# Optimization experiments

Measured on AMD Instinct MI355X. Metric: run time of the kernel, lower is better.

## Reference

```python
import jax, jax.numpy as jnp
import numpy as np

N = 2048
D_T = 256; D_F = 256
E_T = 32; E_F = 32; E_C = 128
C = 5; Q = 512


def setup_inputs() -> dict:
    key = jax.random.key(0)
    ks = jax.random.split(key, 12)
    # full graph minus self-loops, row-major (matches dense_to_sparse ordering)
    r, c = np.meshgrid(np.arange(N), np.arange(N), indexing='ij')
    m = r != c
    edge_index = jnp.asarray(np.stack([r[m], c[m]]), dtype=jnp.int32)  # [2, N*(N-1)]
    E = edge_index.shape[1]
    s = 0.02
    return {
        'time_features': jax.random.normal(ks[0], (N, D_T), jnp.float32),
        'edge_index': edge_index,
        'time_edge_weight': jax.random.uniform(ks[1], (E,), jnp.float32),
        'freq_features': jax.random.normal(ks[2], (N, D_F), jnp.float32),
        'freq_edge_weight': jax.random.uniform(ks[3], (E,), jnp.float32),
        'labels': jax.random.randint(ks[4], (N,), 0, C, jnp.int32),
        'num_classes': C,
        'query_size': Q,
        'Wt': jax.random.normal(ks[5], (D_T, E_T), jnp.float32) * s,
        'bt': jnp.zeros((E_T,), jnp.float32),
        'Wf': jax.random.normal(ks[6], (D_F, E_F), jnp.float32) * s,
        'bf': jnp.zeros((E_F,), jnp.float32),
        'Wc': jax.random.normal(ks[7], (E_T + E_F + C, E_C), jnp.float32) * s,
        'bc': jnp.zeros((E_C,), jnp.float32),
        'Wo': jax.random.normal(ks[8], (E_C, C), jnp.float32) * s,
        'bo': jnp.zeros((C,), jnp.float32),
    }


def _gcn(x, A, W, b):
    # torch_geometric GCNConv: D^{-1/2}(A + I)D^{-1/2} (X W) + b
    n = A.shape[0]
    Ah = A + jnp.eye(n, dtype=A.dtype)
    deg = Ah.sum(axis=1)
    dis = jnp.where(deg > 0, jax.lax.rsqrt(deg), 0.0)
    return (dis[:, None] * Ah * dis[None, :]) @ (x @ W) + b


def reference(time_features, edge_index, time_edge_weight, freq_features,
              freq_edge_weight, labels, num_classes, query_size,
              Wt, bt, Wf, bf, Wc, bc, Wo, bo):
    n = time_features.shape[0]
    lrelu = lambda z: jax.nn.leaky_relu(z, 0.01)

    def dense_adj(w):  # A[dst, src] = w
        return jnp.zeros((n, n), w.dtype).at[edge_index[1], edge_index[0]].add(w)

    te = lrelu(_gcn(time_features, dense_adj(time_edge_weight), Wt, bt))
    fe = lrelu(_gcn(freq_features, dense_adj(freq_edge_weight), Wf, bf))

    # to_one_hot: one_hot[:n - query_size, labels] = 1 -> support rows get 1 in
    # every column that appears anywhere in `labels`
    cols = jnp.zeros((num_classes,), te.dtype).at[labels].set(1.0)
    rowmask = (jnp.arange(n) < (n - query_size)).astype(te.dtype)
    one_hot = rowmask[:, None] * cols[None, :]

    feats = jnp.concatenate([te, fe, one_hot], axis=-1)  # [n, E_T+E_F+C]

    # graph_construction (no_grad in original): 1 / (L1 distance over the
    # non-one-hot dims + 1e-5), zero diagonal
    fd = jax.lax.stop_gradient(feats[:, : feats.shape[1] - num_classes])
    dist = jnp.sum(jnp.abs(fd[:, None, :] - fd[None, :, :]), axis=-1)  # [n, n]
    Aw = (1.0 / (dist + 1e-5)) * (1.0 - jnp.eye(n, dtype=feats.dtype))

    emb = lrelu(_gcn(feats, Aw, Wc, bc))
    return emb @ Wo + bo
```

## Files before the change

kernel.cpp:

```cpp
#include <hip/hip_runtime.h>
#include <hip/hip_bf16.h>

#define N 2048
#define NM1 2047
#define DT 256
#define ET 32
#define EC 128
#define NC 5
#define FS 80
#define FD 69
#define KC_ET 16
#define KC_EC 16

typedef __hip_bfloat16 bf16;
typedef unsigned short u16;
typedef float f32x4 __attribute__((ext_vector_type(4)));
typedef __bf16 bf16x8 __attribute__((ext_vector_type(8)));

__device__ inline u16 bf16_rne(float x){
    unsigned int b = __float_as_uint(x);
    b += 0x7fffu + ((b >> 16) & 1u);
    return (u16)(b >> 16);
}
__device__ inline float bf16_to_f(u16 h){
    return __uint_as_float(((unsigned int)h) << 16);
}

__device__ inline f32x4 mfma16x16x32(bf16x8 a, bf16x8 b, f32x4 c){
    return __builtin_amdgcn_mfma_f32_16x16x32_bf16(a, b, c, 0, 0, 0);
}

__global__ __launch_bounds__(256) void k_deg_label_xw(const float* __restrict__ tw,
                                                      const float* __restrict__ fw,
                                                      const int* __restrict__ labels,
                                                      const float* __restrict__ Xt,
                                                      const float* __restrict__ Wt,
                                                      const float* __restrict__ Xf,
                                                      const float* __restrict__ Wf,
                                                      float* __restrict__ degT,
                                                      float* __restrict__ degF,
                                                      float* __restrict__ cols,
                                                      float* __restrict__ Yt,
                                                      float* __restrict__ Yf){
    int b = blockIdx.x;
    int t = threadIdx.x;
    if (b < 512){
        int p = (b & 7)*256 + t;
        if (p >= NM1) return;
        int s0 = (b >> 3)*32;
        float lowT=0.f, highT=0.f, lowF=0.f, highF=0.f;
        #pragma unroll 8
        for (int r = 0; r < 32; ++r){
            int s = s0 + r;
            float vt = tw[(size_t)s*NM1 + p];
            float vf = fw[(size_t)s*NM1 + p];
            if (s <= p){ highT += vt; highF += vf; }
            else       { lowT  += vt; lowF  += vf; }
        }
        atomicAdd(&degT[p],   lowT);
        atomicAdd(&degF[p],   lowF);
        atomicAdd(&degT[p+1], highT);
        atomicAdd(&degF[p+1], highF);
        return;
    }
    if (b == 512){
        __shared__ float lc[NC];
        if (t < NC) lc[t] = 0.f;
        __syncthreads();
        for (int i = t; i < N; i += 256){
            int l = labels[i];
            if (l >= 0 && l < NC) lc[l] = 1.f;
        }
        __syncthreads();
        if (t < NC) cols[t] = lc[t];
        return;
    }
    int idx = b - 513;
    const float* X = (idx & 256) ? Xf : Xt;
    const float* W = (idx & 256) ? Wf : Wt;
    float*       Y = (idx & 256) ? Yf : Yt;
    __shared__ float Ws[DT*ET];
    __shared__ float Xs[8*DT];
    for (int j = t; j < DT*ET; j += 256) Ws[j] = W[j];
    int i0 = (idx & 255)*8;
    for (int j = t; j < 8*DT; j += 256) Xs[j] = X[(size_t)i0*DT + j];
    __syncthreads();
    int r = t >> 5, f = t & 31;
    const float* xr = Xs + r*DT;
    float acc = 0.f;
    #pragma unroll 8
    for (int d = 0; d < DT; ++d) acc += xr[d]*Ws[d*ET+f];
    Y[(size_t)(i0+r)*ET+f] = acc;
}

__global__ __launch_bounds__(256) void k_agg_et(const float* __restrict__ tw,
                                                const float* __restrict__ fw,
                                                const float* __restrict__ Yt,
                                                const float* __restrict__ Yf,
                                                const float* __restrict__ degT,
                                                const float* __restrict__ degF,
                                                float* __restrict__ Pt,
                                                float* __restrict__ Pf){
    __shared__ float Ast[64*68];
    __shared__ float Asf[64*68];
    __shared__ float Zst[64*ET];
    __shared__ float Zsf[64*ET];
    int t = threadIdx.x;
    int i0 = blockIdx.x*64;
    int kc = blockIdx.y;
    int k0 = kc*128;
    int g  = t >> 7;
    int tt = t & 127;
    int ig = tt >> 3, fg = tt & 7;
    int r0 = ig*4, c0 = fg*4;
    const float* As = g ? Asf : Ast;
    const float* Zs = g ? Zsf : Zst;
    float acc[4][4];
    #pragma unroll
    for (int u=0;u<4;++u)
        #pragma unroll
        for (int v=0;v<4;++v) acc[u][v]=0.f;

    for (int kt = 0; kt < 2; ++kt){
        int kb = k0 + kt*64;
        #pragma unroll
        for (int e = 0; e < 16; ++e){
            int id = t + e*256;
            int k_l = id >> 6, i_l = id & 63;
            int k = kb + k_l;
            int gi = i0 + i_l;
            float vt, vf;
            if (gi == k){ vt = 0.f; vf = 0.f; }
            else {
                size_t base = (size_t)k*NM1 + gi - (gi > k ? 1 : 0);
                vt = tw[base]; vf = fw[base];
            }
            Ast[k_l*68 + i_l] = vt;
            Asf[k_l*68 + i_l] = vf;
        }
        #pragma unroll
        for (int e = 0; e < 2; ++e){
            int id = t + e*256;
            int row = id >> 3;
            int c4  = (id & 7)*4;
            float rdT = rsqrtf(1.f + degT[kb+row]);
            float rdF = rsqrtf(1.f + degF[kb+row]);
            float4 yt = *(const float4*)&Yt[(size_t)(kb+row)*ET + c4];
            float4 yf = *(const float4*)&Yf[(size_t)(kb+row)*ET + c4];
            yt.x*=rdT; yt.y*=rdT; yt.z*=rdT; yt.w*=rdT;
            yf.x*=rdF; yf.y*=rdF; yf.z*=rdF; yf.w*=rdF;
            *(float4*)&Zst[row*ET + c4] = yt;
            *(float4*)&Zsf[row*ET + c4] = yf;
        }
        __syncthreads();
        for (int k = 0; k < 64; ++k){
            float4 a = *(const float4*)&As[k*68 + r0];
            float4 z = *(const float4*)&Zs[k*ET + c0];
            const float* ap = (const float*)&a;
            const float* zp = (const float*)&z;
            #pragma unroll
            for (int u = 0; u < 4; ++u)
                #pragma unroll
                for (int v = 0; v < 4; ++v)
                    acc[u][v] += ap[u]*zp[v];
        }
        __syncthreads();
    }
    float* P = g ? Pf : Pt;
    #pragma unroll
    for (int u = 0; u < 4; ++u){
        size_t ii = (size_t)(i0 + r0 + u);
        float4 o;
        float* po = (float*)&o;
        #pragma unroll
        for (int v = 0; v < 4; ++v) po[v]=acc[u][v];
        *(float4*)&P[(size_t)kc*(N*ET) + ii*ET + c0] = o;
    }
}

__global__ __launch_bounds__(256) void k_feats_epi(const float* __restrict__ Pt,
                                                   const float* __restrict__ Pf,
                                                   const float* __restrict__ Yt,
                                                   const float* __restrict__ Yf,
                                                   const float* __restrict__ degT,
                                                   const float* __restrict__ degF,
                                                   const float* __restrict__ bt,
                                                   const float* __restrict__ bfv,
                                                   const float* __restrict__ cols,
                                                   const int* __restrict__ qsize,
                                                   float* __restrict__ feats){
    int idx = blockIdx.x*256 + threadIdx.x;
    int i = idx >> 6;
    int f = idx & 63;
    float s, rd, b;
    if (f < ET){
        rd = rsqrtf(1.f + degT[i]);
        s = rd*Yt[(size_t)i*ET + f];
        #pragma unroll
        for (int kc = 0; kc < KC_ET; ++kc) s += Pt[(size_t)kc*(N*ET) + (size_t)i*ET + f];
        b = bt[f];
    } else {
        int g = f - ET;
        rd = rsqrtf(1.f + degF[i]);
        s = rd*Yf[(size_t)i*ET + g];
        #pragma unroll
        for (int kc = 0; kc < KC_ET; ++kc) s += Pf[(size_t)kc*(N*ET) + (size_t)i*ET + g];
        b = bfv[g];
    }
    float v = rd*s + b;
    feats[(size_t)i*FS + f] = v > 0.f ? v : 0.01f*v;
    if (f < NC){
        int nsup = N - qsize[0];
        feats[(size_t)i*FS + 2*ET + f] = (i < nsup) ? cols[f] : 0.f;
    }
}

__global__ __launch_bounds__(256) void k_build_aw(const float* __restrict__ feats,
                                                  u16* __restrict__ Aw_hi,
                                                  u16* __restrict__ Aw_lo,
                                                  float* __restrict__ dsum){
    __shared__ float fiT[64*68];
    __shared__ float fjT[64*68];
    int t = threadIdx.x;
    int i0 = blockIdx.x*64, j0 = blockIdx.y*64;
    {
        int row = t >> 2;
        int cb  = (t & 3)*16;
        const float4* si = (const float4*)(feats + (size_t)(i0+row)*FS + cb);
        const float4* sj = (const float4*)(feats + (size_t)(j0+row)*FS + cb);
        #pragma unroll
        for (int s = 0; s < 4; ++s){
            float4 v = si[s];
            float4 w = sj[s];
            int c = cb + s*4;
            fiT[(c+0)*68+row]=v.x; fiT[(c+1)*68+row]=v.y; fiT[(c+2)*68+row]=v.z; fiT[(c+3)*68+row]=v.w;
            fjT[(c+0)*68+row]=w.x; fjT[(c+1)*68+row]=w.y; fjT[(c+2)*68+row]=w.z; fjT[(c+3)*68+row]=w.w;
        }
    }
    __syncthreads();
    int tx = t & 15, ty = t >> 4;
    float acc[4][4];
    #pragma unroll
    for (int u=0;u<4;++u)
        #pragma unroll
        for (int v=0;v<4;++v) acc[u][v]=0.f;
    for (int d = 0; d < 64; ++d){
        float4 a4 = *(const float4*)&fiT[d*68 + ty*4];
        float4 b4 = *(const float4*)&fjT[d*68 + tx*4];
        const float* ap = (const float*)&a4;
        const float* bp = (const float*)&b4;
        #pragma unroll
        for (int u = 0; u < 4; ++u)
            #pragma unroll
            for (int v = 0; v < 4; ++v)
                acc[u][v] += fabsf(ap[u]-bp[v]);
    }
    #pragma unroll
    for (int u = 0; u < 4; ++u){
        int gi = i0 + ty*4 + u;
        float po[4];
        u16 hh[4], ll[4];
        #pragma unroll
        for (int v = 0; v < 4; ++v){
            int gj = j0 + tx*4 + v;
            float w = (gi==gj) ? 1.0f : 1.0f/(acc[u][v] + 1e-5f);
            po[v] = w;
            u16 h = bf16_rne(w);
            hh[v] = h;
            ll[v] = bf16_rne(w - bf16_to_f(h));
        }
        uint2 ph, pl;
        ph.x = (unsigned)hh[0] | ((unsigned)hh[1]<<16);
        ph.y = (unsigned)hh[2] | ((unsigned)hh[3]<<16);
        pl.x = (unsigned)ll[0] | ((unsigned)ll[1]<<16);
        pl.y = (unsigned)ll[2] | ((unsigned)ll[3]<<16);
        *(uint2*)&Aw_hi[(size_t)gi*N + j0 + tx*4] = ph;
        *(uint2*)&Aw_lo[(size_t)gi*N + j0 + tx*4] = pl;
        float rs = (po[0]+po[1]) + (po[2]+po[3]);
        rs += __shfl_xor(rs, 1);
        rs += __shfl_xor(rs, 2);
        rs += __shfl_xor(rs, 4);
        rs += __shfl_xor(rs, 8);
        if (tx == 0) atomicAdd(&dsum[gi], rs);
    }
}

__global__ __launch_bounds__(256) void k_featswc(const float* __restrict__ feats,
                                                 const float* __restrict__ Wc,
                                                 const float* __restrict__ dsum,
                                                 u16* __restrict__ ZcT_hi,
                                                 u16* __restrict__ ZcT_lo){
    __shared__ float Wcs[FD*EC];
    __shared__ float fr[8][FD+3];
    __shared__ float zb[128][12];
    int t = threadIdx.x;
    for (int idx = t; idx < FD*EC; idx += 256) Wcs[idx] = Wc[idx];
    int i0 = blockIdx.x*8;
    for (int idx = t; idx < 8*FD; idx += 256){
        int r = idx / FD;
        int c = idx - r*FD;
        fr[r][c] = feats[(size_t)(i0+r)*FS + c];
    }
    __syncthreads();
    int f  = t & 127;
    int rh = t >> 7;
    for (int rr = 0; rr < 4; ++rr){
        int r = rh*4 + rr;
        float acc = 0.f;
        #pragma unroll
        for (int d = 0; d < FD; ++d) acc += fr[r][d]*Wcs[d*EC+f];
        int i = i0 + r;
        zb[f][r] = rsqrtf(dsum[i])*acc;
    }
    __syncthreads();
    int p = rh, f2 = f;
    float4 v0 = *(const float4*)&zb[f2][0];
    float4 v1 = *(const float4*)&zb[f2][4];
    float vv[8] = {v0.x, v0.y, v0.z, v0.w, v1.x, v1.y, v1.z, v1.w};
    u16 s[8];
    #pragma unroll
    for (int j = 0; j < 8; ++j){
        u16 h = bf16_rne(vv[j]);
        s[j] = p ? bf16_rne(vv[j] - bf16_to_f(h)) : h;
    }
    uint4 pk;
    pk.x = (unsigned)s[0] | ((unsigned)s[1]<<16);
    pk.y = (unsigned)s[2] | ((unsigned)s[3]<<16);
    pk.z = (unsigned)s[4] | ((unsigned)s[5]<<16);
    pk.w = (unsigned)s[6] | ((unsigned)s[7]<<16);
    u16* dst = p ? ZcT_lo : ZcT_hi;
    *(uint4*)&dst[(size_t)f2*N + i0] = pk;
}

__global__ __launch_bounds__(256) void k_agg_ec(const u16* __restrict__ Aw_hi,
                                                const u16* __restrict__ Aw_lo,
                                                const u16* __restrict__ ZcT_hi,
                                                const u16* __restrict__ ZcT_lo,
                                                float* __restrict__ Pe){
    __shared__ u16 Ah[64*72];
    __shared__ u16 Al[64*72];
    __shared__ u16 Zh[128*72];
    __shared__ u16 Zl[128*72];
    int t = threadIdx.x;
    int w  = t >> 6;
    int l  = t & 63;
    int lr = l & 15;
    int lg = l >> 4;
    int i0 = blockIdx.x*64;
    int kb0 = blockIdx.y*128;
    f32x4 acc[8];
    #pragma unroll
    for (int tt = 0; tt < 8; ++tt) acc[tt] = (f32x4){0.f, 0.f, 0.f, 0.f};

    for (int sub = 0; sub < 2; ++sub){
        int kbs = kb0 + sub*64;
        #pragma unroll
        for (int e = 0; e < 2; ++e){
            int id = t + e*256;
            int row = id >> 3, ch = (id & 7)*8;
            uint4 vh = *(const uint4*)&Aw_hi[(size_t)(i0+row)*N + kbs + ch];
            uint4 vl = *(const uint4*)&Aw_lo[(size_t)(i0+row)*N + kbs + ch];
            *(uint4*)&Ah[row*72 + ch] = vh;
            *(uint4*)&Al[row*72 + ch] = vl;
        }
        #pragma unroll
        for (int e = 0; e < 4; ++e){
            int id = t + e*256;
            int row = id >> 3, ch = (id & 7)*8;
            uint4 vh = *(const uint4*)&ZcT_hi[(size_t)row*N + kbs + ch];
            uint4 vl = *(const uint4*)&ZcT_lo[(size_t)row*N + kbs + ch];
            *(uint4*)&Zh[row*72 + ch] = vh;
            *(uint4*)&Zl[row*72 + ch] = vl;
        }
        __syncthreads();
        #pragma unroll
        for (int ks = 0; ks < 2; ++ks){
            int aoff = (w*16 + lr)*72 + ks*32 + lg*8;
            bf16x8 aH = *(const bf16x8*)&Ah[aoff];
            bf16x8 aL = *(const bf16x8*)&Al[aoff];
            #pragma unroll
            for (int tt = 0; tt < 8; ++tt){
                int zoff = (tt*16 + lr)*72 + ks*32 + lg*8;
                bf16x8 bH = *(const bf16x8*)&Zh[zoff];
                bf16x8 bL = *(const bf16x8*)&Zl[zoff];
                acc[tt] = mfma16x16x32(aH, bH, acc[tt]);
                acc[tt] = mfma16x16x32(aL, bH, acc[tt]);
                acc[tt] = mfma16x16x32(aH, bL, acc[tt]);
            }
        }
        __syncthreads();
    }
    float* pout = Pe + (size_t)blockIdx.y*((size_t)N*EC);
    #pragma unroll
    for (int tt = 0; tt < 8; ++tt){
        #pragma unroll
        for (int r = 0; r < 4; ++r){
            int gi = i0 + w*16 + lg*4 + r;
            pout[(size_t)gi*EC + tt*16 + lr] = acc[tt][r];
        }
    }
}

__global__ __launch_bounds__(256) void k_embfinal(const float* __restrict__ Pe,
                                                  const float* __restrict__ dsum,
                                                  const float* __restrict__ bc,
                                                  const float* __restrict__ Wo,
                                                  const float* __restrict__ bo,
                                                  float* __restrict__ out){
    __shared__ float vs[2][EC];
    __shared__ float Wos[EC*NC];
    __shared__ float bos[NC];
    int t = threadIdx.x;
    for (int idx = t; idx < EC*NC; idx += 256) Wos[idx] = Wo[idx];
    if (t < NC) bos[t] = bo[t];
    int rr = t >> 7, f = t & 127;
    int i = blockIdx.x*2 + rr;
    size_t idx = (size_t)i*EC + f;
    float s = 0.f;
    #pragma unroll
    for (int kc = 0; kc < KC_EC; ++kc) s += Pe[(size_t)kc*(N*EC) + idx];
    float v = rsqrtf(dsum[i])*s + bc[f];
    vs[rr][f] = v > 0.f ? v : 0.01f*v;
    __syncthreads();
    if (t < 2*NC){
        int r = t / NC;
        int c = t - r*NC;
        float a = bos[c];
        #pragma unroll 8
        for (int f2 = 0; f2 < EC; ++f2) a += vs[r][f2]*Wos[f2*NC+c];
        out[(size_t)(blockIdx.x*2 + r)*NC + c] = a;
    }
}

extern "C" void kernel_launch(void* const* d_in, const int* in_sizes, int n_in,
                              void* d_out, int out_size, void* d_ws, size_t ws_size,
                              hipStream_t stream) {
    const float* time_features = (const float*)d_in[0];
    const float* tw            = (const float*)d_in[2];
    const float* freq_features = (const float*)d_in[3];
    const float* fw            = (const float*)d_in[4];
    const int*   labels        = (const int*)d_in[5];
    const int*   qsize         = (const int*)d_in[7];
    const float* Wt  = (const float*)d_in[8];
    const float* bt  = (const float*)d_in[9];
    const float* Wf  = (const float*)d_in[10];
    const float* bfv = (const float*)d_in[11];
    const float* Wc  = (const float*)d_in[12];
    const float* bc  = (const float*)d_in[13];
    const float* Wo  = (const float*)d_in[14];
    const float* bo  = (const float*)d_in[15];
    float* out = (float*)d_out;

    float* ws    = (float*)d_ws;
    float* Yt    = ws;
    float* Yf    = Yt + (size_t)N*ET;
    float* Zc    = Yf + (size_t)N*ET;
    float* degT  = Zc + (size_t)N*EC;
    float* degF  = degT + N;
    float* dsum  = degF + N;
    float* colsb = dsum + N;
    float* feats = colsb + 8;
    float* Aw    = feats + (size_t)N*FS;
    float* Pt    = Aw + (size_t)N*N;
    float* Pf    = Pt + (size_t)KC_ET*N*ET;
    float* Pe    = Pf + (size_t)KC_ET*N*ET;

    u16* Aw_hi  = (u16*)Aw;
    u16* Aw_lo  = Aw_hi + (size_t)N*N;
    u16* ZcT_hi = (u16*)Zc;
    u16* ZcT_lo = ZcT_hi + (size_t)N*EC;

    hipMemsetAsync(degT, 0, 3*N*sizeof(float), stream);
    k_deg_label_xw<<<1025, 256, 0, stream>>>(tw, fw, labels,
                                             time_features, Wt, freq_features, Wf,
                                             degT, degF, colsb, Yt, Yf);
    k_agg_et<<<dim3(N/64, KC_ET), 256, 0, stream>>>(tw, fw, Yt, Yf, degT, degF, Pt, Pf);
    k_feats_epi<<<(N*64)/256, 256, 0, stream>>>(Pt, Pf, Yt, Yf, degT, degF,
                                                bt, bfv, colsb, qsize, feats);
    k_build_aw<<<dim3(N/64, N/64), 256, 0, stream>>>(feats, Aw_hi, Aw_lo, dsum);
    k_featswc<<<N/8, 256, 0, stream>>>(feats, Wc, dsum, ZcT_hi, ZcT_lo);
    k_agg_ec<<<dim3(N/64, KC_EC), 256, 0, stream>>>(Aw_hi, Aw_lo, ZcT_hi, ZcT_lo, Pe);
    k_embfinal<<<N/2, 256, 0, stream>>>(Pe, dsum, bc, Wo, bo, out);
}
```

Before: 199.8 us.

## Fuse split-K GCN aggregations with epilogues, drop partial buffers, use MFMA for first stage

The first-layer aggregation moves from FP32 FMA to split-bf16 MFMA (hi/lo, three products). It drops split-K, so each block covers 16 rows over the full K range, and the bias, leaky-ReLU and feats epilogue are fused in. The second aggregation is likewise made full-K per 16-row block and fused with the final embedding and output projection, removing the Pe partial-sum buffer and two kernel launches. The trade-off is far fewer blocks (256 and 128) with long serial K loops and less parallelism, which could leave much of the GPU idle.

Result: slower. 264.6 us (+32.4%).

```diff
diff --git a/kernel.cpp b/kernel.cpp
--- a/kernel.cpp
+++ b/kernel.cpp
@@ -9,10 +9,7 @@
 #define NC 5
 #define FS 80
 #define FD 69
-#define KC_ET 16
-#define KC_EC 16
-
-typedef __hip_bfloat16 bf16;
+
 typedef unsigned short u16;
 typedef float f32x4 __attribute__((ext_vector_type(4)));
 typedef __bf16 bf16x8 __attribute__((ext_vector_type(8)));
@@ -25,7 +22,6 @@
 __device__ inline float bf16_to_f(u16 h){
     return __uint_as_float(((unsigned int)h) << 16);
 }
-
 __device__ inline f32x4 mfma16x16x32(bf16x8 a, bf16x8 b, f32x4 c){
     return __builtin_amdgcn_mfma_f32_16x16x32_bf16(a, b, c, 0, 0, 0);
 }
@@ -93,125 +89,85 @@
     Y[(size_t)(i0+r)*ET+f] = acc;
 }
 
-__global__ __launch_bounds__(256) void k_agg_et(const float* __restrict__ tw,
-                                                const float* __restrict__ fw,
-                                                const float* __restrict__ Yt,
-                                                const float* __restrict__ Yf,
-                                                const float* __restrict__ degT,
-                                                const float* __restrict__ degF,
-                                                float* __restrict__ Pt,
-                                                float* __restrict__ Pf){
-    __shared__ float Ast[64*68];
-    __shared__ float Asf[64*68];
-    __shared__ float Zst[64*ET];
-    __shared__ float Zsf[64*ET];
+__global__ __launch_bounds__(256) void k_agg_et_full(const float* __restrict__ tw,
+                                                     const float* __restrict__ fw,
+                                                     const float* __restrict__ Yt,
+                                                     const float* __restrict__ Yf,
+                                                     const float* __restrict__ degT,
+                                                     const float* __restrict__ degF,
+                                                     const float* __restrict__ bt,
+                                                     const float* __restrict__ bfv,
+                                                     const float* __restrict__ cols,
+                                                     const int* __restrict__ qsize,
+                                                     float* __restrict__ feats){
+    __shared__ u16 Ah[16*72], Al[16*72];
+    __shared__ u16 Zh[32*72], Zl[32*72];
+    __shared__ float red[256*4];
     int t = threadIdx.x;
-    int i0 = blockIdx.x*64;
-    int kc = blockIdx.y;
-    int k0 = kc*128;
-    int g  = t >> 7;
-    int tt = t & 127;
-    int ig = tt >> 3, fg = tt & 7;
-    int r0 = ig*4, c0 = fg*4;
-    const float* As = g ? Asf : Ast;
-    const float* Zs = g ? Zsf : Zst;
-    float acc[4][4];
-    #pragma unroll
-    for (int u=0;u<4;++u)
-        #pragma unroll
-        for (int v=0;v<4;++v) acc[u][v]=0.f;
-
-    for (int kt = 0; kt < 2; ++kt){
-        int kb = k0 + kt*64;
-        #pragma unroll
-        for (int e = 0; e < 16; ++e){
+    int tile = blockIdx.x >> 1;
+    int g = blockIdx.x & 1;
+    int i0 = tile*16;
+    const float* A   = g ? fw   : tw;
+    const float* Y   = g ? Yf   : Yt;
+    const float* deg = g ? degF : degT;
+    int w = t >> 6, l = t & 63, lr = l & 15, lg = l >> 4;
+    int cf = w & 1, kp = w >> 1;
+    f32x4 acc = {0.f, 0.f, 0.f, 0.f};
+
+    for (int sub = 0; sub < 32; ++sub){
+        int kb = sub*64;
+        #pragma unroll
+        for (int e = 0; e < 4; ++e){
             int id = t + e*256;
-            int k_l = id >> 6, i_l = id & 63;
-            int k = kb + k_l;
-            int gi = i0 + i_l;
-            float vt, vf;
-            if (gi == k){ vt = 0.f; vf = 0.f; }
-            else {
-                size_t base = (size_t)k*NM1 + gi - (gi > k ? 1 : 0);
-                vt = tw[base]; vf = fw[base];
-            }
-            Ast[k_l*68 + i_l] = vt;
-            Asf[k_l*68 + i_l] = vf;
-        }
-        #pragma unroll
-        for (int e = 0; e < 2; ++e){
+            int i_l = id & 15, k_l = id >> 4;
+            int gi = i0 + i_l, k = kb + k_l;
+            float v = 0.f;
+            if (gi != k) v = A[(size_t)k*NM1 + gi - (gi > k ? 1 : 0)];
+            u16 h = bf16_rne(v);
+            Ah[i_l*72 + k_l] = h;
+            Al[i_l*72 + k_l] = bf16_rne(v - bf16_to_f(h));
+        }
+        #pragma unroll
+        for (int e = 0; e < 8; ++e){
             int id = t + e*256;
-            int row = id >> 3;
-            int c4  = (id & 7)*4;
-            float rdT = rsqrtf(1.f + degT[kb+row]);
-            float rdF = rsqrtf(1.f + degF[kb+row]);
-            float4 yt = *(const float4*)&Yt[(size_t)(kb+row)*ET + c4];
-            float4 yf = *(const float4*)&Yf[(size_t)(kb+row)*ET + c4];
-            yt.x*=rdT; yt.y*=rdT; yt.z*=rdT; yt.w*=rdT;
-            yf.x*=rdF; yf.y*=rdF; yf.z*=rdF; yf.w*=rdF;
-            *(float4*)&Zst[row*ET + c4] = yt;
-            *(float4*)&Zsf[row*ET + c4] = yf;
-        }
-        __syncthreads();
-        for (int k = 0; k < 64; ++k){
-            float4 a = *(const float4*)&As[k*68 + r0];
-            float4 z = *(const float4*)&Zs[k*ET + c0];
-            const float* ap = (const float*)&a;
-            const float* zp = (const float*)&z;
-            #pragma unroll
-            for (int u = 0; u < 4; ++u)
-                #pragma unroll
-                for (int v = 0; v < 4; ++v)
-                    acc[u][v] += ap[u]*zp[v];
-        }
-        __syncthreads();
-    }
-    float* P = g ? Pf : Pt;
-    #pragma unroll
-    for (int u = 0; u < 4; ++u){
-        size_t ii = (size_t)(i0 + r0 + u);
-        float4 o;
-        float* po = (float*)&o;
-        #pragma unroll
-        for (int v = 0; v < 4; ++v) po[v]=acc[u][v];
-        *(float4*)&P[(size_t)kc*(N*ET) + ii*ET + c0] = o;
-    }
-}
-
-__global__ __launch_bounds__(256) void k_feats_epi(const float* __restrict__ Pt,
-                                                   const float* __restrict__ Pf,
-                                                   const float* __restrict__ Yt,
-                                                   const float* __restrict__ Yf,
-                                                   const float* __restrict__ degT,
-                                                   const float* __restrict__ degF,
-                                                   const float* __restrict__ bt,
-                                                   const float* __restrict__ bfv,
-                                                   const float* __restrict__ cols,
-                                                   const int* __restrict__ qsize,
-                                                   float* __restrict__ feats){
-    int idx = blockIdx.x*256 + threadIdx.x;
-    int i = idx >> 6;
-    int f = idx & 63;
-    float s, rd, b;
-    if (f < ET){
-        rd = rsqrtf(1.f + degT[i]);
-        s = rd*Yt[(size_t)i*ET + f];
-        #pragma unroll
-        for (int kc = 0; kc < KC_ET; ++kc) s += Pt[(size_t)kc*(N*ET) + (size_t)i*ET + f];
-        b = bt[f];
-    } else {
-        int g = f - ET;
-        rd = rsqrtf(1.f + degF[i]);
-        s = rd*Yf[(size_t)i*ET + g];
-        #pragma unroll
-        for (int kc = 0; kc < KC_ET; ++kc) s += Pf[(size_t)kc*(N*ET) + (size_t)i*ET + g];
-        b = bfv[g];
-    }
-    float v = rd*s + b;
-    feats[(size_t)i*FS + f] = v > 0.f ? v : 0.01f*v;
-    if (f < NC){
+            int f = id & 31, k_l = id >> 5;
+            float rd = rsqrtf(1.f + deg[kb + k_l]);
+            float v = rd * Y[(size_t)(kb+k_l)*ET + f];
+            u16 h = bf16_rne(v);
+            Zh[f*72 + k_l] = h;
+            Zl[f*72 + k_l] = bf16_rne(v - bf16_to_f(h));
+        }
+        __syncthreads();
+        int aoff = lr*72 + kp*32 + lg*8;
+        int boff = (cf*16 + lr)*72 + kp*32 + lg*8;
+        bf16x8 aH = *(const bf16x8*)&Ah[aoff];
+        bf16x8 aL = *(const bf16x8*)&Al[aoff];
+        bf16x8 bH = *(const bf16x8*)&Zh[boff];
+        bf16x8 bL = *(const bf16x8*)&Zl[boff];
+        acc = mfma16x16x32(aH, bH, acc);
+        acc = mfma16x16x32(aL, bH, acc);
+        acc = mfma16x16x32(aH, bL, acc);
+        __syncthreads();
+    }
+    *(f32x4*)&red[t*4] = acc;
+    __syncthreads();
+    if (w < 2){
+        f32x4 o = *(const f32x4*)&red[(t+128)*4];
+        int fl = cf*16 + lr;
+        float bb = g ? bfv[fl] : bt[fl];
+        #pragma unroll
+        for (int j = 0; j < 4; ++j){
+            int i = i0 + lg*4 + j;
+            float rd = rsqrtf(1.f + deg[i]);
+            float s = rd*Y[(size_t)i*ET + fl] + acc[j] + o[j];
+            float v = rd*s + bb;
+            feats[(size_t)i*FS + g*ET + fl] = v > 0.f ? v : 0.01f*v;
+        }
+    }
+    if (g == 0 && t < 16*NC){
+        int r = t / NC, c = t - r*NC;
         int nsup = N - qsize[0];
-        feats[(size_t)i*FS + 2*ET + f] = (i < nsup) ? cols[f] : 0.f;
+        feats[(size_t)(i0+r)*FS + 2*ET + c] = (i0+r < nsup) ? cols[c] : 0.f;
     }
 }
 
@@ -332,103 +288,76 @@
     *(uint4*)&dst[(size_t)f2*N + i0] = pk;
 }
 
-__global__ __launch_bounds__(256) void k_agg_ec(const u16* __restrict__ Aw_hi,
-                                                const u16* __restrict__ Aw_lo,
-                                                const u16* __restrict__ ZcT_hi,
-                                                const u16* __restrict__ ZcT_lo,
-                                                float* __restrict__ Pe){
-    __shared__ u16 Ah[64*72];
-    __shared__ u16 Al[64*72];
-    __shared__ u16 Zh[128*72];
-    __shared__ u16 Zl[128*72];
+__global__ __launch_bounds__(256) void k_agg_ec_full(const u16* __restrict__ Aw_hi,
+                                                     const u16* __restrict__ Aw_lo,
+                                                     const u16* __restrict__ ZcT_hi,
+                                                     const u16* __restrict__ ZcT_lo,
+                                                     const float* __restrict__ dsum,
+                                                     const float* __restrict__ bc,
+                                                     const float* __restrict__ Wo,
+                                                     const float* __restrict__ bo,
+                                                     float* __restrict__ out){
+    __shared__ u16 Ah[16*72], Al[16*72];
+    __shared__ u16 Zh[128*72], Zl[128*72];
+    __shared__ float vs[16*128];
     int t = threadIdx.x;
-    int w  = t >> 6;
-    int l  = t & 63;
-    int lr = l & 15;
-    int lg = l >> 4;
-    int i0 = blockIdx.x*64;
-    int kb0 = blockIdx.y*128;
-    f32x4 acc[8];
-    #pragma unroll
-    for (int tt = 0; tt < 8; ++tt) acc[tt] = (f32x4){0.f, 0.f, 0.f, 0.f};
-
-    for (int sub = 0; sub < 2; ++sub){
-        int kbs = kb0 + sub*64;
-        #pragma unroll
-        for (int e = 0; e < 2; ++e){
-            int id = t + e*256;
-            int row = id >> 3, ch = (id & 7)*8;
-            uint4 vh = *(const uint4*)&Aw_hi[(size_t)(i0+row)*N + kbs + ch];
-            uint4 vl = *(const uint4*)&Aw_lo[(size_t)(i0+row)*N + kbs + ch];
-            *(uint4*)&Ah[row*72 + ch] = vh;
-            *(uint4*)&Al[row*72 + ch] = vl;
+    int i0 = blockIdx.x*16;
+    int w = t >> 6, l = t & 63, lr = l & 15, lg = l >> 4;
+    f32x4 acc0 = {0.f,0.f,0.f,0.f}, acc1 = {0.f,0.f,0.f,0.f};
+
+    for (int sub = 0; sub < 32; ++sub){
+        int kb = sub*64;
+        {
+            int row = t >> 4, c4 = (t & 15)*4;
+            *(uint2*)&Ah[row*72 + c4] = *(const uint2*)&Aw_hi[(size_t)(i0+row)*N + kb + c4];
+            *(uint2*)&Al[row*72 + c4] = *(const uint2*)&Aw_lo[(size_t)(i0+row)*N + kb + c4];
         }
         #pragma unroll
         for (int e = 0; e < 4; ++e){
             int id = t + e*256;
-            int row = id >> 3, ch = (id & 7)*8;
-            uint4 vh = *(const uint4*)&ZcT_hi[(size_t)row*N + kbs + ch];
-            uint4 vl = *(const uint4*)&ZcT_lo[(size_t)row*N + kbs + ch];
-            *(uint4*)&Zh[row*72 + ch] = vh;
-            *(uint4*)&Zl[row*72 + ch] = vl;
+            int fr = id >> 3, ch = (id & 7)*8;
+            *(uint4*)&Zh[fr*72 + ch] = *(const uint4*)&ZcT_hi[(size_t)fr*N + kb + ch];
+            *(uint4*)&Zl[fr*72 + ch] = *(const uint4*)&ZcT_lo[(size_t)fr*N + kb + ch];
         }
         __syncthreads();
         #pragma unroll
         for (int ks = 0; ks < 2; ++ks){
-            int aoff = (w*16 + lr)*72 + ks*32 + lg*8;
+            int aoff = lr*72 + ks*32 + lg*8;
             bf16x8 aH = *(const bf16x8*)&Ah[aoff];
             bf16x8 aL = *(const bf16x8*)&Al[aoff];
-            #pragma unroll
-            for (int tt = 0; tt < 8; ++tt){
-                int zoff = (tt*16 + lr)*72 + ks*32 + lg*8;
-                bf16x8 bH = *(const bf16x8*)&Zh[zoff];
-                bf16x8 bL = *(const bf16x8*)&Zl[zoff];
-                acc[tt] = mfma16x16x32(aH, bH, acc[tt]);
-                acc[tt] = mfma16x16x32(aL, bH, acc[tt]);
-                acc[tt] = mfma16x16x32(aH, bL, acc[tt]);
-            }
-        }
-        __syncthreads();
-    }
-    float* pout = Pe + (size_t)blockIdx.y*((size_t)N*EC);
+            int b0 = ((w*2+0)*16 + lr)*72 + ks*32 + lg*8;
+            int b1 = ((w*2+1)*16 + lr)*72 + ks*32 + lg*8;
+            bf16x8 bH0 = *(const bf16x8*)&Zh[b0];
+            bf16x8 bL0 = *(const bf16x8*)&Zl[b0];
+            bf16x8 bH1 = *(const bf16x8*)&Zh[b1];
+            bf16x8 bL1 = *(const bf16x8*)&Zl[b1];
+            acc0 = mfma16x16x32(aH, bH0, acc0);
+            acc0 = mfma16x16x32(aL, bH0, acc0);
+            acc0 = mfma16x16x32(aH, bL0, acc0);
+            acc1 = mfma16x16x32(aH, bH1, acc1);
+            acc1 = mfma16x16x32(aL, bH1, acc1);
+            acc1 = mfma16x16x32(aH, bL1, acc1);
+        }
+        __syncthreads();
+    }
     #pragma unroll
-    for (int tt = 0; tt < 8; ++tt){
-        #pragma unroll
-        for (int r = 0; r < 4; ++r){
-            int gi = i0 + w*16 + lg*4 + r;
-            pout[(size_t)gi*EC + tt*16 + lr] = acc[tt][r];
-        }
-    }
-}
-
-__global__ __launch_bounds__(256) void k_embfinal(const float* __restrict__ Pe,
-                                                  const float* __restrict__ dsum,
-                                                  const float* __restrict__ bc,
-                                                  const float* __restrict__ Wo,
-                                                  const float* __restrict__ bo,
-                                                  float* __restrict__ out){
-    __shared__ float vs[2][EC];
-    __shared__ float Wos[EC*NC];
-    __shared__ float bos[NC];
-    int t = threadIdx.x;
-    for (int idx = t; idx < EC*NC; idx += 256) Wos[idx] = Wo[idx];
-    if (t < NC) bos[t] = bo[t];
-    int rr = t >> 7, f = t & 127;
-    int i = blockIdx.x*2 + rr;
-    size_t idx = (size_t)i*EC + f;
-    float s = 0.f;
-    #pragma unroll
-    for (int kc = 0; kc < KC_EC; ++kc) s += Pe[(size_t)kc*(N*EC) + idx];
-    float v = rsqrtf(dsum[i])*s + bc[f];
-    vs[rr][f] = v > 0.f ? v : 0.01f*v;
-    __syncthreads();
-    if (t < 2*NC){
-        int r = t / NC;
-        int c = t - r*NC;
-        float a = bos[c];
+    for (int j = 0; j < 4; ++j){
+        int row = lg*4 + j;
+        float rdv = rsqrtf(dsum[i0+row]);
+        int c0 = (w*2+0)*16 + lr;
+        int c1 = (w*2+1)*16 + lr;
+        float v0 = rdv*acc0[j] + bc[c0];
+        float v1 = rdv*acc1[j] + bc[c1];
+        vs[row*128 + c0] = v0 > 0.f ? v0 : 0.01f*v0;
+        vs[row*128 + c1] = v1 > 0.f ? v1 : 0.01f*v1;
+    }
+    __syncthreads();
+    if (t < 16*NC){
+        int r = t / NC, c = t - r*NC;
+        float a = bo[c];
         #pragma unroll 8
-        for (int f2 = 0; f2 < EC; ++f2) a += vs[r][f2]*Wos[f2*NC+c];
-        out[(size_t)(blockIdx.x*2 + r)*NC + c] = a;
+        for (int f = 0; f < EC; ++f) a += vs[r*128 + f]*Wo[f*NC + c];
+        out[(size_t)(i0 + r)*NC + c] = a;
     }
 }
 
@@ -452,33 +381,29 @@
     float* out = (float*)d_out;
 
     float* ws    = (float*)d_ws;
-    float* Yt    = ws;
-    float* Yf    = Yt + (size_t)N*ET;
-    float* Zc    = Yf + (size_t)N*ET;
-    float* degT  = Zc + (size_t)N*EC;
+    float* degT  = ws;
     float* degF  = degT + N;
     float* dsum  = degF + N;
     float* colsb = dsum + N;
-    float* feats = colsb + 8;
-    float* Aw    = feats + (size_t)N*FS;
-    float* Pt    = Aw + (size_t)N*N;
-    float* Pf    = Pt + (size_t)KC_ET*N*ET;
-    float* Pe    = Pf + (size_t)KC_ET*N*ET;
-
+    float* Yt    = colsb + 8;
+    float* Yf    = Yt + (size_t)N*ET;
+    float* feats = Yf + (size_t)N*ET;
+    float* Zc    = feats + (size_t)N*FS;
+    float* Aw    = Zc + (size_t)N*EC;
+
+    u16* ZcT_hi = (u16*)Zc;
+    u16* ZcT_lo = ZcT_hi + (size_t)N*EC;
     u16* Aw_hi  = (u16*)Aw;
     u16* Aw_lo  = Aw_hi + (size_t)N*N;
-    u16* ZcT_hi = (u16*)Zc;
-    u16* ZcT_lo = ZcT_hi + (size_t)N*EC;
 
     hipMemsetAsync(degT, 0, 3*N*sizeof(float), stream);
     k_deg_label_xw<<<1025, 256, 0, stream>>>(tw, fw, labels,
                                              time_features, Wt, freq_features, Wf,
                                              degT, degF, colsb, Yt, Yf);
-    k_agg_et<<<dim3(N/64, KC_ET), 256, 0, stream>>>(tw, fw, Yt, Yf, degT, degF, Pt, Pf);
-    k_feats_epi<<<(N*64)/256, 256, 0, stream>>>(Pt, Pf, Yt, Yf, degT, degF,
-                                                bt, bfv, colsb, qsize, feats);
+    k_agg_et_full<<<256, 256, 0, stream>>>(tw, fw, Yt, Yf, degT, degF,
+                                           bt, bfv, colsb, qsize, feats);
     k_build_aw<<<dim3(N/64, N/64), 256, 0, stream>>>(feats, Aw_hi, Aw_lo, dsum);
     k_featswc<<<N/8, 256, 0, stream>>>(feats, Wc, dsum, ZcT_hi, ZcT_lo);
-    k_agg_ec<<<dim3(N/64, KC_EC), 256, 0, stream>>>(Aw_hi, Aw_lo, ZcT_hi, ZcT_lo, Pe);
-    k_embfinal<<<N/2, 256, 0, stream>>>(Pe, dsum, bc, Wo, bo, out);
-}
+    k_agg_ec_full<<<128, 256, 0, stream>>>(Aw_hi, Aw_lo, ZcT_hi, ZcT_lo,
+                                           dsum, bc, Wo, bo, out);
+}
```

## Use split-bf16 MFMA for edge aggregation and fuse Aw build with feats·Wc

Applied to the files above, without the earlier changes.

Rewrites the time/frequency adjacency aggregation to use bf16 hi/lo split MFMA instead of scalar FP32 FMAs, reading adjacency directly from global memory into registers. Merges the Aw distance kernel and the feats·Wc kernel into one launch. To allow that merge, the rsqrt(dsum) column scaling moves out of Zc and into k_agg_ec's A-tile load, where each Aw element is recombined, rescaled and re-split. This saves a launch and uses matrix cores, but adds extra conversion ALU work in k_agg_ec, and the 3-term split may slightly change precision.

Result: faster. 191.1 us (-4.4%).

```diff
diff --git a/kernel.cpp b/kernel.cpp
--- a/kernel.cpp
+++ b/kernel.cpp
@@ -12,7 +12,6 @@
 #define KC_ET 16
 #define KC_EC 16
 
-typedef __hip_bfloat16 bf16;
 typedef unsigned short u16;
 typedef float f32x4 __attribute__((ext_vector_type(4)));
 typedef __bf16 bf16x8 __attribute__((ext_vector_type(8)));
@@ -25,7 +24,6 @@
 __device__ inline float bf16_to_f(u16 h){
     return __uint_as_float(((unsigned int)h) << 16);
 }
-
 __device__ inline f32x4 mfma16x16x32(bf16x8 a, bf16x8 b, f32x4 c){
     return __builtin_amdgcn_mfma_f32_16x16x32_bf16(a, b, c, 0, 0, 0);
 }
@@ -93,89 +91,122 @@
     Y[(size_t)(i0+r)*ET+f] = acc;
 }
 
-__global__ __launch_bounds__(256) void k_agg_et(const float* __restrict__ tw,
-                                                const float* __restrict__ fw,
-                                                const float* __restrict__ Yt,
-                                                const float* __restrict__ Yf,
-                                                const float* __restrict__ degT,
-                                                const float* __restrict__ degF,
-                                                float* __restrict__ Pt,
-                                                float* __restrict__ Pf){
-    __shared__ float Ast[64*68];
-    __shared__ float Asf[64*68];
-    __shared__ float Zst[64*ET];
-    __shared__ float Zsf[64*ET];
+__global__ __launch_bounds__(256) void k_agg_et_m(const float* __restrict__ tw,
+                                                  const float* __restrict__ fw,
+                                                  const float* __restrict__ Yt,
+                                                  const float* __restrict__ Yf,
+                                                  const float* __restrict__ degT,
+                                                  const float* __restrict__ degF,
+                                                  float* __restrict__ Pt,
+                                                  float* __restrict__ Pf){
+    __shared__ u16 Zs[2][2][32][136];
     int t = threadIdx.x;
+    int w = t >> 6, l = t & 63, lr = l & 15, lg = l >> 4;
+    int g = w >> 1, wh = w & 1;
     int i0 = blockIdx.x*64;
     int kc = blockIdx.y;
     int k0 = kc*128;
-    int g  = t >> 7;
-    int tt = t & 127;
-    int ig = tt >> 3, fg = tt & 7;
-    int r0 = ig*4, c0 = fg*4;
-    const float* As = g ? Asf : Ast;
-    const float* Zs = g ? Zsf : Zst;
-    float acc[4][4];
+
+    {
+        int f = t >> 3;
+        int kb16 = (t & 7)*16;
+        #pragma unroll
+        for (int gg = 0; gg < 2; ++gg){
+            const float* Y   = gg ? Yf   : Yt;
+            const float* deg = gg ? degF : degT;
+            u16 h8[16], l8[16];
+            #pragma unroll
+            for (int j = 0; j < 16; ++j){
+                int k = k0 + kb16 + j;
+                float rd = rsqrtf(1.f + deg[k]);
+                float v = rd * Y[(size_t)k*ET + f];
+                u16 h = bf16_rne(v);
+                h8[j] = h;
+                l8[j] = bf16_rne(v - bf16_to_f(h));
+            }
+            uint4 pk;
+            pk.x = (unsigned)h8[0] | ((unsigned)h8[1]<<16);
+            pk.y = (unsigned)h8[2] | ((unsigned)h8[3]<<16);
+            pk.z = (unsigned)h8[4] | ((unsigned)h8[5]<<16);
+            pk.w = (unsigned)h8[6] | ((unsigned)h8[7]<<16);
+            *(uint4*)&Zs[gg][0][f][kb16] = pk;
+            pk.x = (unsigned)h8[8] | ((unsigned)h8[9]<<16);
+            pk.y = (unsigned)h8[10] | ((unsigned)h8[11]<<16);
+            pk.z = (unsigned)h8[12] | ((unsigned)h8[13]<<16);
+            pk.w = (unsigned)h8[14] | ((unsigned)h8[15]<<16);
+            *(uint4*)&Zs[gg][0][f][kb16+8] = pk;
+            pk.x = (unsigned)l8[0] | ((unsigned)l8[1]<<16);
+            pk.y = (unsigned)l8[2] | ((unsigned)l8[3]<<16);
+            pk.z = (unsigned)l8[4] | ((unsigned)l8[5]<<16);
+            pk.w = (unsigned)l8[6] | ((unsigned)l8[7]<<16);
+            *(uint4*)&Zs[gg][1][f][kb16] = pk;
+            pk.x = (unsigned)l8[8] | ((unsigned)l8[9]<<16);
+            pk.y = (unsigned)l8[10] | ((unsigned)l8[11]<<16);
+            pk.z = (unsigned)l8[12] | ((unsigned)l8[13]<<16);
+            pk.w = (unsigned)l8[14] | ((unsigned)l8[15]<<16);
+            *(uint4*)&Zs[gg][1][f][kb16+8] = pk;
+        }
+    }
+    __syncthreads();
+
+    const float* A = g ? fw : tw;
+    f32x4 acc[2][2];
     #pragma unroll
-    for (int u=0;u<4;++u)
-        #pragma unroll
-        for (int v=0;v<4;++v) acc[u][v]=0.f;
-
-    for (int kt = 0; kt < 2; ++kt){
-        int kb = k0 + kt*64;
-        #pragma unroll
-        for (int e = 0; e < 16; ++e){
-            int id = t + e*256;
-            int k_l = id >> 6, i_l = id & 63;
-            int k = kb + k_l;
-            int gi = i0 + i_l;
-            float vt, vf;
-            if (gi == k){ vt = 0.f; vf = 0.f; }
-            else {
-                size_t base = (size_t)k*NM1 + gi - (gi > k ? 1 : 0);
-                vt = tw[base]; vf = fw[base];
-            }
-            Ast[k_l*68 + i_l] = vt;
-            Asf[k_l*68 + i_l] = vf;
-        }
-        #pragma unroll
-        for (int e = 0; e < 2; ++e){
-            int id = t + e*256;
-            int row = id >> 3;
-            int c4  = (id & 7)*4;
-            float rdT = rsqrtf(1.f + degT[kb+row]);
-            float rdF = rsqrtf(1.f + degF[kb+row]);
-            float4 yt = *(const float4*)&Yt[(size_t)(kb+row)*ET + c4];
-            float4 yf = *(const float4*)&Yf[(size_t)(kb+row)*ET + c4];
-            yt.x*=rdT; yt.y*=rdT; yt.z*=rdT; yt.w*=rdT;
-            yf.x*=rdF; yf.y*=rdF; yf.z*=rdF; yf.w*=rdF;
-            *(float4*)&Zst[row*ET + c4] = yt;
-            *(float4*)&Zsf[row*ET + c4] = yf;
-        }
-        __syncthreads();
-        for (int k = 0; k < 64; ++k){
-            float4 a = *(const float4*)&As[k*68 + r0];
-            float4 z = *(const float4*)&Zs[k*ET + c0];
-            const float* ap = (const float*)&a;
-            const float* zp = (const float*)&z;
-            #pragma unroll
-            for (int u = 0; u < 4; ++u)
+    for (int fi = 0; fi < 2; ++fi)
+        #pragma unroll
+        for (int ff = 0; ff < 2; ++ff) acc[fi][ff] = (f32x4){0.f,0.f,0.f,0.f};
+
+    for (int sub = 0; sub < 2; ++sub){
+        int kb = k0 + sub*64;
+        #pragma unroll
+        for (int fi = 0; fi < 2; ++fi){
+            int row = i0 + wh*32 + fi*16 + lr;
+            #pragma unroll
+            for (int ks = 0; ks < 2; ++ks){
+                int kbase = kb + ks*32 + lg*8;
+                u16 ah[8], al[8];
                 #pragma unroll
-                for (int v = 0; v < 4; ++v)
-                    acc[u][v] += ap[u]*zp[v];
-        }
-        __syncthreads();
+                for (int j = 0; j < 8; ++j){
+                    int k = kbase + j;
+                    float v = 0.f;
+                    if (row != k) v = A[(size_t)k*NM1 + row - (row > k ? 1 : 0)];
+                    u16 h = bf16_rne(v);
+                    ah[j] = h;
+                    al[j] = bf16_rne(v - bf16_to_f(h));
+                }
+                uint4 pa, pb;
+                pa.x = (unsigned)ah[0] | ((unsigned)ah[1]<<16);
+                pa.y = (unsigned)ah[2] | ((unsigned)ah[3]<<16);
+                pa.z = (unsigned)ah[4] | ((unsigned)ah[5]<<16);
+                pa.w = (unsigned)ah[6] | ((unsigned)ah[7]<<16);
+                pb.x = (unsigned)al[0] | ((unsigned)al[1]<<16);
+                pb.y = (unsigned)al[2] | ((unsigned)al[3]<<16);
+                pb.z = (unsigned)al[4] | ((unsigned)al[5]<<16);
+                pb.w = (unsigned)al[6] | ((unsigned)al[7]<<16);
+                bf16x8 aH = *(bf16x8*)&pa;
+                bf16x8 aL = *(bf16x8*)&pb;
+                int koff = sub*64 + ks*32 + lg*8;
+                #pragma unroll
+                for (int ff = 0; ff < 2; ++ff){
+                    bf16x8 bH = *(const bf16x8*)&Zs[g][0][ff*16+lr][koff];
+                    bf16x8 bL = *(const bf16x8*)&Zs[g][1][ff*16+lr][koff];
+                    acc[fi][ff] = mfma16x16x32(aH, bH, acc[fi][ff]);
+                    acc[fi][ff] = mfma16x16x32(aL, bH, acc[fi][ff]);
+                    acc[fi][ff] = mfma16x16x32(aH, bL, acc[fi][ff]);
+                }
+            }
+        }
     }
     float* P = g ? Pf : Pt;
     #pragma unroll
-    for (int u = 0; u < 4; ++u){
-        size_t ii = (size_t)(i0 + r0 + u);
-        float4 o;
-        float* po = (float*)&o;
-        #pragma unroll
-        for (int v = 0; v < 4; ++v) po[v]=acc[u][v];
-        *(float4*)&P[(size_t)kc*(N*ET) + ii*ET + c0] = o;
-    }
+    for (int fi = 0; fi < 2; ++fi)
+        #pragma unroll
+        for (int ff = 0; ff < 2; ++ff)
+            #pragma unroll
+            for (int r = 0; r < 4; ++r){
+                int gi = i0 + wh*32 + fi*16 + lg*4 + r;
+                P[(size_t)kc*(N*ET) + (size_t)gi*ET + ff*16 + lr] = acc[fi][ff][r];
+            }
 }
 
 __global__ __launch_bounds__(256) void k_feats_epi(const float* __restrict__ Pt,
@@ -215,127 +246,122 @@
     }
 }
 
-__global__ __launch_bounds__(256) void k_build_aw(const float* __restrict__ feats,
-                                                  u16* __restrict__ Aw_hi,
-                                                  u16* __restrict__ Aw_lo,
-                                                  float* __restrict__ dsum){
-    __shared__ float fiT[64*68];
-    __shared__ float fjT[64*68];
+__global__ __launch_bounds__(256) void k_aw_zc(const float* __restrict__ feats,
+                                               const float* __restrict__ Wc,
+                                               u16* __restrict__ Aw_hi,
+                                               u16* __restrict__ Aw_lo,
+                                               u16* __restrict__ ZcT_hi,
+                                               u16* __restrict__ ZcT_lo,
+                                               float* __restrict__ dsum){
+    __shared__ __align__(16) char sm[37632];
     int t = threadIdx.x;
-    int i0 = blockIdx.x*64, j0 = blockIdx.y*64;
+    int b = blockIdx.x;
+    if (b < 1024){
+        float* fiT = (float*)sm;
+        float* fjT = fiT + 64*68;
+        int i0 = (b & 31)*64, j0 = (b >> 5)*64;
+        {
+            int row = t >> 2;
+            int cb  = (t & 3)*16;
+            const float4* si = (const float4*)(feats + (size_t)(i0+row)*FS + cb);
+            const float4* sj = (const float4*)(feats + (size_t)(j0+row)*FS + cb);
+            #pragma unroll
+            for (int s = 0; s < 4; ++s){
+                float4 v = si[s];
+                float4 w = sj[s];
+                int c = cb + s*4;
+                fiT[(c+0)*68+row]=v.x; fiT[(c+1)*68+row]=v.y; fiT[(c+2)*68+row]=v.z; fiT[(c+3)*68+row]=v.w;
+                fjT[(c+0)*68+row]=w.x; fjT[(c+1)*68+row]=w.y; fjT[(c+2)*68+row]=w.z; fjT[(c+3)*68+row]=w.w;
+            }
+        }
+        __syncthreads();
+        int tx = t & 15, ty = t >> 4;
+        float acc[4][4];
+        #pragma unroll
+        for (int u=0;u<4;++u)
+            #pragma unroll
+            for (int v=0;v<4;++v) acc[u][v]=0.f;
+        for (int d = 0; d < 64; ++d){
+            float4 a4 = *(const float4*)&fiT[d*68 + ty*4];
+            float4 b4 = *(const float4*)&fjT[d*68 + tx*4];
+            const float* ap = (const float*)&a4;
+            const float* bp = (const float*)&b4;
+            #pragma unroll
+            for (int u = 0; u < 4; ++u)
+                #pragma unroll
+                for (int v = 0; v < 4; ++v)
+                    acc[u][v] += fabsf(ap[u]-bp[v]);
+        }
+        #pragma unroll
+        for (int u = 0; u < 4; ++u){
+            int gi = i0 + ty*4 + u;
+            float po[4];
+            u16 hh[4], ll[4];
+            #pragma unroll
+            for (int v = 0; v < 4; ++v){
+                int gj = j0 + tx*4 + v;
+                float w = (gi==gj) ? 1.0f : 1.0f/(acc[u][v] + 1e-5f);
+                po[v] = w;
+                u16 h = bf16_rne(w);
+                hh[v] = h;
+                ll[v] = bf16_rne(w - bf16_to_f(h));
+            }
+            uint2 ph, pl;
+            ph.x = (unsigned)hh[0] | ((unsigned)hh[1]<<16);
+            ph.y = (unsigned)hh[2] | ((unsigned)hh[3]<<16);
+            pl.x = (unsigned)ll[0] | ((unsigned)ll[1]<<16);
+            pl.y = (unsigned)ll[2] | ((unsigned)ll[3]<<16);
+            *(uint2*)&Aw_hi[(size_t)gi*N + j0 + tx*4] = ph;
+            *(uint2*)&Aw_lo[(size_t)gi*N + j0 + tx*4] = pl;
+            float rs = (po[0]+po[1]) + (po[2]+po[3]);
+            rs += __shfl_xor(rs, 1);
+            rs += __shfl_xor(rs, 2);
+            rs += __shfl_xor(rs, 4);
+            rs += __shfl_xor(rs, 8);
+            if (tx == 0) atomicAdd(&dsum[gi], rs);
+        }
+        return;
+    }
     {
-        int row = t >> 2;
-        int cb  = (t & 3)*16;
-        const float4* si = (const float4*)(feats + (size_t)(i0+row)*FS + cb);
-        const float4* sj = (const float4*)(feats + (size_t)(j0+row)*FS + cb);
-        #pragma unroll
-        for (int s = 0; s < 4; ++s){
-            float4 v = si[s];
-            float4 w = sj[s];
-            int c = cb + s*4;
-            fiT[(c+0)*68+row]=v.x; fiT[(c+1)*68+row]=v.y; fiT[(c+2)*68+row]=v.z; fiT[(c+3)*68+row]=v.w;
-            fjT[(c+0)*68+row]=w.x; fjT[(c+1)*68+row]=w.y; fjT[(c+2)*68+row]=w.z; fjT[(c+3)*68+row]=w.w;
-        }
-    }
-    __syncthreads();
-    int tx = t & 15, ty = t >> 4;
-    float acc[4][4];
-    #pragma unroll
-    for (int u=0;u<4;++u)
-        #pragma unroll
-        for (int v=0;v<4;++v) acc[u][v]=0.f;
-    for (int d = 0; d < 64; ++d){
-        float4 a4 = *(const float4*)&fiT[d*68 + ty*4];
-        float4 b4 = *(const float4*)&fjT[d*68 + tx*4];
-        const float* ap = (const float*)&a4;
-        const float* bp = (const float*)&b4;
-        #pragma unroll
-        for (int u = 0; u < 4; ++u)
-            #pragma unroll
-            for (int v = 0; v < 4; ++v)
-                acc[u][v] += fabsf(ap[u]-bp[v]);
-    }
-    #pragma unroll
-    for (int u = 0; u < 4; ++u){
-        int gi = i0 + ty*4 + u;
-        float po[4];
+        float* Wcs = (float*)sm;
+        float* fr  = Wcs + FD*EC;
+        int idx = b - 1024;
+        int i0 = idx*8;
+        for (int j = t; j < FD*EC; j += 256) Wcs[j] = Wc[j];
+        for (int j = t; j < 8*FD; j += 256){
+            int r = j / FD;
+            int c = j - r*FD;
+            fr[r*72 + c] = feats[(size_t)(i0+r)*FS + c];
+        }
+        __syncthreads();
+        int f  = t & 127;
+        int rh = t >> 7;
         u16 hh[4], ll[4];
         #pragma unroll
-        for (int v = 0; v < 4; ++v){
-            int gj = j0 + tx*4 + v;
-            float w = (gi==gj) ? 1.0f : 1.0f/(acc[u][v] + 1e-5f);
-            po[v] = w;
-            u16 h = bf16_rne(w);
-            hh[v] = h;
-            ll[v] = bf16_rne(w - bf16_to_f(h));
+        for (int rr = 0; rr < 4; ++rr){
+            int r = rh*4 + rr;
+            float acc = 0.f;
+            #pragma unroll
+            for (int d = 0; d < FD; ++d) acc += fr[r*72+d]*Wcs[d*EC+f];
+            u16 h = bf16_rne(acc);
+            hh[rr] = h;
+            ll[rr] = bf16_rne(acc - bf16_to_f(h));
         }
         uint2 ph, pl;
         ph.x = (unsigned)hh[0] | ((unsigned)hh[1]<<16);
         ph.y = (unsigned)hh[2] | ((unsigned)hh[3]<<16);
         pl.x = (unsigned)ll[0] | ((unsigned)ll[1]<<16);
         pl.y = (unsigned)ll[2] | ((unsigned)ll[3]<<16);
-        *(uint2*)&Aw_hi[(size_t)gi*N + j0 + tx*4] = ph;
-        *(uint2*)&Aw_lo[(size_t)gi*N + j0 + tx*4] = pl;
-        float rs = (po[0]+po[1]) + (po[2]+po[3]);
-        rs += __shfl_xor(rs, 1);
-        rs += __shfl_xor(rs, 2);
-        rs += __shfl_xor(rs, 4);
-        rs += __shfl_xor(rs, 8);
-        if (tx == 0) atomicAdd(&dsum[gi], rs);
-    }
-}
-
-__global__ __launch_bounds__(256) void k_featswc(const float* __restrict__ feats,
-                                                 const float* __restrict__ Wc,
-                                                 const float* __restrict__ dsum,
-                                                 u16* __restrict__ ZcT_hi,
-                                                 u16* __restrict__ ZcT_lo){
-    __shared__ float Wcs[FD*EC];
-    __shared__ float fr[8][FD+3];
-    __shared__ float zb[128][12];
-    int t = threadIdx.x;
-    for (int idx = t; idx < FD*EC; idx += 256) Wcs[idx] = Wc[idx];
-    int i0 = blockIdx.x*8;
-    for (int idx = t; idx < 8*FD; idx += 256){
-        int r = idx / FD;
-        int c = idx - r*FD;
-        fr[r][c] = feats[(size_t)(i0+r)*FS + c];
-    }
-    __syncthreads();
-    int f  = t & 127;
-    int rh = t >> 7;
-    for (int rr = 0; rr < 4; ++rr){
-        int r = rh*4 + rr;
-        float acc = 0.f;
-        #pragma unroll
-        for (int d = 0; d < FD; ++d) acc += fr[r][d]*Wcs[d*EC+f];
-        int i = i0 + r;
-        zb[f][r] = rsqrtf(dsum[i])*acc;
-    }
-    __syncthreads();
-    int p = rh, f2 = f;
-    float4 v0 = *(const float4*)&zb[f2][0];
-    float4 v1 = *(const float4*)&zb[f2][4];
-    float vv[8] = {v0.x, v0.y, v0.z, v0.w, v1.x, v1.y, v1.z, v1.w};
-    u16 s[8];
-    #pragma unroll
-    for (int j = 0; j < 8; ++j){
-        u16 h = bf16_rne(vv[j]);
-        s[j] = p ? bf16_rne(vv[j] - bf16_to_f(h)) : h;
-    }
-    uint4 pk;
-    pk.x = (unsigned)s[0] | ((unsigned)s[1]<<16);
-    pk.y = (unsigned)s[2] | ((unsigned)s[3]<<16);
-    pk.z = (unsigned)s[4] | ((unsigned)s[5]<<16);
-    pk.w = (unsigned)s[6] | ((unsigned)s[7]<<16);
-    u16* dst = p ? ZcT_lo : ZcT_hi;
-    *(uint4*)&dst[(size_t)f2*N + i0] = pk;
+        *(uint2*)&ZcT_hi[(size_t)f*N + i0 + rh*4] = ph;
+        *(uint2*)&ZcT_lo[(size_t)f*N + i0 + rh*4] = pl;
+    }
 }
 
 __global__ __launch_bounds__(256) void k_agg_ec(const u16* __restrict__ Aw_hi,
                                                 const u16* __restrict__ Aw_lo,
                                                 const u16* __restrict__ ZcT_hi,
                                                 const u16* __restrict__ ZcT_lo,
+                                                const float* __restrict__ dsum,
                                                 float* __restrict__ Pe){
     __shared__ u16 Ah[64*72];
     __shared__ u16 Al[64*72];
@@ -360,8 +386,28 @@
             int row = id >> 3, ch = (id & 7)*8;
             uint4 vh = *(const uint4*)&Aw_hi[(size_t)(i0+row)*N + kbs + ch];
             uint4 vl = *(const uint4*)&Aw_lo[(size_t)(i0+row)*N + kbs + ch];
-            *(uint4*)&Ah[row*72 + ch] = vh;
-            *(uint4*)&Al[row*72 + ch] = vl;
+            const u16* ph = (const u16*)&vh;
+            const u16* pl = (const u16*)&vl;
+            u16 nh[8], nl[8];
+            #pragma unroll
+            for (int j = 0; j < 8; ++j){
+                float a = bf16_to_f(ph[j]) + bf16_to_f(pl[j]);
+                float v = a * rsqrtf(dsum[kbs + ch + j]);
+                u16 h = bf16_rne(v);
+                nh[j] = h;
+                nl[j] = bf16_rne(v - bf16_to_f(h));
+            }
+            uint4 oh, ol;
+            oh.x = (unsigned)nh[0] | ((unsigned)nh[1]<<16);
+            oh.y = (unsigned)nh[2] | ((unsigned)nh[3]<<16);
+            oh.z = (unsigned)nh[4] | ((unsigned)nh[5]<<16);
+            oh.w = (unsigned)nh[6] | ((unsigned)nh[7]<<16);
+            ol.x = (unsigned)nl[0] | ((unsigned)nl[1]<<16);
+            ol.y = (unsigned)nl[2] | ((unsigned)nl[3]<<16);
+            ol.z = (unsigned)nl[4] | ((unsigned)nl[5]<<16);
+            ol.w = (unsigned)nl[6] | ((unsigned)nl[7]<<16);
+            *(uint4*)&Ah[row*72 + ch] = oh;
+            *(uint4*)&Al[row*72 + ch] = ol;
         }
         #pragma unroll
         for (int e = 0; e < 4; ++e){
@@ -390,13 +436,12 @@
         }
         __syncthreads();
     }
-    float* pout = Pe + (size_t)blockIdx.y*((size_t)N*EC);
     #pragma unroll
     for (int tt = 0; tt < 8; ++tt){
         #pragma unroll
         for (int r = 0; r < 4; ++r){
             int gi = i0 + w*16 + lg*4 + r;
-            pout[(size_t)gi*EC + tt*16 + lr] = acc[tt][r];
+            Pe[(size_t)blockIdx.y*(N*EC) + (size_t)gi*EC + tt*16 + lr] = acc[tt][r];
         }
     }
 }
@@ -452,33 +497,32 @@
     float* out = (float*)d_out;
 
     float* ws    = (float*)d_ws;
-    float* Yt    = ws;
-    float* Yf    = Yt + (size_t)N*ET;
-    float* Zc    = Yf + (size_t)N*ET;
-    float* degT  = Zc + (size_t)N*EC;
+    float* degT  = ws;
     float* degF  = degT + N;
     float* dsum  = degF + N;
     float* colsb = dsum + N;
-    float* feats = colsb + 8;
-    float* Aw    = feats + (size_t)N*FS;
+    float* Yt    = colsb + 8;
+    float* Yf    = Yt + (size_t)N*ET;
+    float* feats = Yf + (size_t)N*ET;
+    float* Zc    = feats + (size_t)N*FS;
+    float* Aw    = Zc + (size_t)N*EC;
     float* Pt    = Aw + (size_t)N*N;
     float* Pf    = Pt + (size_t)KC_ET*N*ET;
     float* Pe    = Pf + (size_t)KC_ET*N*ET;
 
+    u16* ZcT_hi = (u16*)Zc;
+    u16* ZcT_lo = ZcT_hi + (size_t)N*EC;
     u16* Aw_hi  = (u16*)Aw;
     u16* Aw_lo  = Aw_hi + (size_t)N*N;
-    u16* ZcT_hi = (u16*)Zc;
-    u16* ZcT_lo = ZcT_hi + (size_t)N*EC;
 
     hipMemsetAsync(degT, 0, 3*N*sizeof(float), stream);
     k_deg_label_xw<<<1025, 256, 0, stream>>>(tw, fw, labels,
                                              time_features, Wt, freq_features, Wf,
                                              degT, degF, colsb, Yt, Yf);
-    k_agg_et<<<dim3(N/64, KC_ET), 256, 0, stream>>>(tw, fw, Yt, Yf, degT, degF, Pt, Pf);
+    k_agg_et_m<<<dim3(N/64, KC_ET), 256, 0, stream>>>(tw, fw, Yt, Yf, degT, degF, Pt, Pf);
     k_feats_epi<<<(N*64)/256, 256, 0, stream>>>(Pt, Pf, Yt, Yf, degT, degF,
                                                 bt, bfv, colsb, qsize, feats);
-    k_build_aw<<<dim3(N/64, N/64), 256, 0, stream>>>(feats, Aw_hi, Aw_lo, dsum);
-    k_featswc<<<N/8, 256, 0, stream>>>(feats, Wc, dsum, ZcT_hi, ZcT_lo);
-    k_agg_ec<<<dim3(N/64, KC_EC), 256, 0, stream>>>(Aw_hi, Aw_lo, ZcT_hi, ZcT_lo, Pe);
+    k_aw_zc<<<1280, 256, 0, stream>>>(feats, Wc, Aw_hi, Aw_lo, ZcT_hi, ZcT_lo, dsum);
+    k_agg_ec<<<dim3(N/64, KC_EC), 256, 0, stream>>>(Aw_hi, Aw_lo, ZcT_hi, ZcT_lo, dsum, Pe);
     k_embfinal<<<N/2, 256, 0, stream>>>(Pe, dsum, bc, Wo, bo, out);
 }
```
